# Optimization experiments

Hardware: AMD Instinct MI355X
Metric: run time of the kernel (lower is better)

## Reference

```python
import jax, jax.numpy as jnp
import numpy as np

B, N = 32, 2048
NUM_FEATURE, NUM_CLUSTER, D_MODEL = 512, 256, 1024
LN_EPS = 1e-5
NEG_SLOPE = 0.2


def setup_inputs() -> dict:
    key = jax.random.key(0)
    ks = jax.random.split(key, 8)
    s_feat = 1.0 / np.sqrt(NUM_FEATURE)
    s_city = 1.0 / np.sqrt(NUM_CLUSTER)
    return {
        "input": jax.random.normal(ks[0], (B, N, NUM_FEATURE), dtype=jnp.float32),
        "static": jax.random.normal(ks[1], (N, NUM_CLUSTER), dtype=jnp.float32),
        # torch.nn.Linear stores weight as [out, in]
        "W_feat": jax.random.uniform(ks[2], (D_MODEL, NUM_FEATURE), jnp.float32, -s_feat, s_feat),
        "b_feat": jax.random.uniform(ks[3], (D_MODEL,), jnp.float32, -s_feat, s_feat),
        "W_city": jax.random.uniform(ks[4], (D_MODEL, NUM_CLUSTER), jnp.float32, -s_city, s_city),
        "b_city": jax.random.uniform(ks[5], (D_MODEL,), jnp.float32, -s_city, s_city),
        "gamma": jnp.ones((D_MODEL,), dtype=jnp.float32),
        "beta": jnp.zeros((D_MODEL,), dtype=jnp.float32),
    }


def reference(input, static, W_feat, b_feat, W_city, b_city, gamma, beta):
    # x = leaky_relu(feat_embed(input), 0.2)  -> [B, N, d_model]
    x = jnp.einsum("bnf,df->bnd", input, W_feat) + b_feat
    x = jnp.where(x >= 0, x, NEG_SLOPE * x)
    # c = city_embed(static) -> [N, d_model]; diag_embed + matmul == elementwise gate
    c = jnp.einsum("nk,dk->nd", static, W_city) + b_city
    x = x * c[None, :, :]
    # LayerNorm over d_model (eps=1e-5, elementwise affine)
    mu = jnp.mean(x, axis=-1, keepdims=True)
    var = jnp.mean(jnp.square(x - mu), axis=-1, keepdims=True)
    x = (x - mu) * jax.lax.rsqrt(var + LN_EPS)
    return x * gamma + beta
```

## Files before the change

kernel.cpp:

```cpp
#include <hip/hip_runtime.h>
#include <hip/hip_bf16.h>


typedef __attribute__((ext_vector_type(8))) short short8;
typedef __attribute__((ext_vector_type(4))) float f32x4;

__device__ __forceinline__ unsigned short f2bf(float f) {
    unsigned int u = __float_as_uint(f);
    return (unsigned short)((u + 0x7FFFu + ((u >> 16) & 1u)) >> 16);
}
__device__ __forceinline__ float b2f(unsigned short h) {
    return __uint_as_float(((unsigned int)h) << 16);
}

__global__ __launch_bounds__(256) void convw_kernel(
    const float* __restrict__ w, unsigned short* __restrict__ o)
{
    int gid = blockIdx.x * 256 + threadIdx.x;
    int idx = gid * 4;
    int row = idx >> 9;
    int k   = idx & 511;
    float4 v = *(const float4*)(w + idx);
    uint2 p;
    p.x = (unsigned)f2bf(v.x) | ((unsigned)f2bf(v.y) << 16);
    p.y = (unsigned)f2bf(v.z) | ((unsigned)f2bf(v.w) << 16);
    int dst = ((k >> 5) << 15) + (row << 5) + (k & 31);
    *(uint2*)(o + dst) = p;
}

__global__ __launch_bounds__(256) void city_kernel(
    const float* __restrict__ st,
    const float* __restrict__ Wc,
    const float* __restrict__ bc,
    unsigned short* __restrict__ cg)
{
    __shared__ __align__(16) unsigned short Sa[64 * 264];
    __shared__ __align__(16) unsigned short Sb[128 * 264];
    const int t  = threadIdx.x;
    const int n0 = blockIdx.x << 6;
    const int d0 = blockIdx.y << 7;

    #pragma unroll
    for (int i = 0; i < 16; ++i) {
        int idx = (i << 8) + t;
        int row = idx >> 6, kq = (idx & 63) << 2;
        float4 v = *(const float4*)(st + (size_t)(n0 + row) * 256 + kq);
        uint2 p;
        p.x = (unsigned)f2bf(v.x) | ((unsigned)f2bf(v.y) << 16);
        p.y = (unsigned)f2bf(v.z) | ((unsigned)f2bf(v.w) << 16);
        *(uint2*)(Sa + row * 264 + kq) = p;
    }
    #pragma unroll
    for (int i = 0; i < 32; ++i) {
        int idx = (i << 8) + t;
        int row = idx >> 6, kq = (idx & 63) << 2;
        float4 v = *(const float4*)(Wc + (size_t)(d0 + row) * 256 + kq);
        uint2 p;
        p.x = (unsigned)f2bf(v.x) | ((unsigned)f2bf(v.y) << 16);
        p.y = (unsigned)f2bf(v.z) | ((unsigned)f2bf(v.w) << 16);
        *(uint2*)(Sb + row * 264 + kq) = p;
    }
    __syncthreads();

    const int wv = t >> 6;
    const int cl = t & 15, q = (t >> 4) & 3;
    f32x4 acc[4][2];
    #pragma unroll
    for (int rt = 0; rt < 4; ++rt)
        #pragma unroll
        for (int ct = 0; ct < 2; ++ct) acc[rt][ct] = (f32x4)0.f;

    #pragma unroll
    for (int ks = 0; ks < 8; ++ks) {
        short8 a[4];
        #pragma unroll
        for (int rt = 0; rt < 4; ++rt)
            a[rt] = *(const short8*)(Sa + ((rt << 4) + cl) * 264 + (ks << 5) + (q << 3));
        #pragma unroll
        for (int ct = 0; ct < 2; ++ct) {
            short8 bf8 = *(const short8*)(Sb + ((wv << 5) + (ct << 4) + cl) * 264 + (ks << 5) + (q << 3));
            #pragma unroll
            for (int rt = 0; rt < 4; ++rt)
                acc[rt][ct] = __builtin_amdgcn_mfma_f32_16x16x32_bf16(a[rt], bf8, acc[rt][ct], 0, 0, 0);
        }
    }
    #pragma unroll
    for (int ct = 0; ct < 2; ++ct) {
        const int d = d0 + (wv << 5) + (ct << 4) + cl;
        const float bcv = bc[d];
        #pragma unroll
        for (int rt = 0; rt < 4; ++rt)
            #pragma unroll
            for (int rr = 0; rr < 4; ++rr) {
                const int row = (rt << 4) + (q << 2) + rr;
                cg[(size_t)(n0 + row) * 1024 + d] = f2bf(acc[rt][ct][rr] + bcv);
            }
    }
}

__global__ __launch_bounds__(1024, 4) void feat_kernel(
    const float* __restrict__ inp,
    const unsigned short* __restrict__ Wr,
    const float* __restrict__ b_feat,
    const unsigned short* __restrict__ cg,
    const float* __restrict__ gamma,
    const float* __restrict__ beta,
    float* __restrict__ out)
{
    __shared__ __align__(16) unsigned short As[64 * 520];
    __shared__ float red1[16 * 64];
    __shared__ float red2[16 * 64];
    __shared__ float smu[64];
    __shared__ float srs[64];

    const int t    = threadIdx.x;
    const int lane = t & 63;
    const int w    = t >> 6;
    const int cl   = lane & 15;
    const int q    = lane >> 4;
    const int m0   = blockIdx.x << 6;
    const int n0   = m0 & 2047;

    f32x4 acc[4][4];
    #pragma unroll
    for (int rt = 0; rt < 4; ++rt)
        #pragma unroll
        for (int ct = 0; ct < 4; ++ct) acc[rt][ct] = (f32x4)0.f;

    const unsigned short* bp = Wr + ((((w << 6) + cl) << 5) + (q << 3));

    short8 bc[4], bn[4];
    #pragma unroll
    for (int ct = 0; ct < 4; ++ct)
        bc[ct] = *(const short8*)(bp + (ct << 9));

    {
        const float* ag = inp + (size_t)m0 * 512;
        #pragma unroll
        for (int j = 0; j < 8; ++j) {
            int g = (j << 10) + t;
            float4 v = *(const float4*)(ag + ((size_t)g << 2));
            int row = g >> 7, c4 = g & 127;
            uint2 p;
            p.x = (unsigned)f2bf(v.x) | ((unsigned)f2bf(v.y) << 16);
            p.y = (unsigned)f2bf(v.z) | ((unsigned)f2bf(v.w) << 16);
            *(uint2*)(&As[row * 520 + (c4 << 2)]) = p;
        }
    }
    __syncthreads();

    const int abase = cl * 520 + (q << 3);
    #pragma unroll
    for (int kb = 0; kb < 16; ++kb) {
        if (kb < 15) {
            #pragma unroll
            for (int ct = 0; ct < 4; ++ct)
                bn[ct] = *(const short8*)(bp + ((kb + 1) << 15) + (ct << 9));
        }
        short8 a[4];
        #pragma unroll
        for (int rt = 0; rt < 4; ++rt)
            a[rt] = *(const short8*)(&As[abase + rt * (16 * 520) + (kb << 5)]);
        #pragma unroll
        for (int ct = 0; ct < 4; ++ct)
            #pragma unroll
            for (int rt = 0; rt < 4; ++rt)
                acc[rt][ct] = __builtin_amdgcn_mfma_f32_16x16x32_bf16(a[rt], bc[ct], acc[rt][ct], 0, 0, 0);
        if (kb < 15) {
            #pragma unroll
            for (int ct = 0; ct < 4; ++ct) bc[ct] = bn[ct];
        }
    }

    float bfv[4];
    #pragma unroll
    for (int ct = 0; ct < 4; ++ct) bfv[ct] = b_feat[(w << 6) + (ct << 4) + cl];

    #pragma unroll
    for (int rt = 0; rt < 4; ++rt) {
        #pragma unroll
        for (int rr = 0; rr < 4; ++rr) {
            const int row = (rt << 4) + (q << 2) + rr;
            float s1 = 0.f, s2 = 0.f;
            #pragma unroll
            for (int ct = 0; ct < 4; ++ct) {
                const int d = (w << 6) + (ct << 4) + cl;
                float x = acc[rt][ct][rr] + bfv[ct];
                x = (x >= 0.f) ? x : 0.2f * x;
                x *= b2f(cg[(size_t)(n0 + row) * 1024 + d]);
                acc[rt][ct][rr] = x;
                s1 += x;
                s2 += x * x;
            }
            #pragma unroll
            for (int off = 1; off < 16; off <<= 1) {
                s1 += __shfl_xor(s1, off, 64);
                s2 += __shfl_xor(s2, off, 64);
            }
            if (cl == 0) {
                red1[(w << 6) + row] = s1;
                red2[(w << 6) + row] = s2;
            }
        }
    }
    __syncthreads();
    if (t < 64) {
        float a = 0.f, bb = 0.f;
        #pragma unroll
        for (int j = 0; j < 16; ++j) { a += red1[(j << 6) + t]; bb += red2[(j << 6) + t]; }
        const float mu  = a * (1.0f / 1024.0f);
        const float var = bb * (1.0f / 1024.0f) - mu * mu;
        smu[t] = mu;
        srs[t] = rsqrtf(var + 1e-5f);
    }
    __syncthreads();

    #pragma unroll
    for (int ct = 0; ct < 4; ++ct) {
        const int d = (w << 6) + (ct << 4) + cl;
        const float g = gamma[d], be = beta[d];
        #pragma unroll
        for (int rt = 0; rt < 4; ++rt) {
            #pragma unroll
            for (int rr = 0; rr < 4; ++rr) {
                const int row = (rt << 4) + (q << 2) + rr;
                __builtin_nontemporal_store(
                    (acc[rt][ct][rr] - smu[row]) * srs[row] * g + be,
                    &out[(size_t)(m0 + row) * 1024 + d]);
            }
        }
    }
}

extern "C" void kernel_launch(void* const* d_in, const int* in_sizes, int n_in,
                              void* d_out, int out_size, void* d_ws, size_t ws_size,
                              hipStream_t stream) {
    const float* inp   = (const float*)d_in[0];
    const float* st    = (const float*)d_in[1];
    const float* Wf    = (const float*)d_in[2];
    const float* bfeat = (const float*)d_in[3];
    const float* Wc    = (const float*)d_in[4];
    const float* bc    = (const float*)d_in[5];
    const float* gamma = (const float*)d_in[6];
    const float* beta  = (const float*)d_in[7];
    float* out = (float*)d_out;

    unsigned short* wsWr = (unsigned short*)d_ws;
    unsigned short* wsC  = (unsigned short*)((char*)d_ws + (1 << 20));

    convw_kernel<<<512, 256, 0, stream>>>(Wf, wsWr);
    city_kernel<<<dim3(32, 8), 256, 0, stream>>>(st, Wc, bc, wsC);
    feat_kernel<<<1024, 1024, 0, stream>>>(inp, wsWr, bfeat, wsC, gamma, beta, out);
}
```

Baseline: 486.2 us.

## Double-buffer A and W tiles in LDS via async global_load_lds

The feat kernel no longer converts the whole 64x512 input tile to bf16 in LDS up front, and no longer prefetches W through registers. It now streams both the fp32 input chunk and the bf16 weight chunk per k-step into double-buffered LDS using the asynchronous global_load_lds builtin, with an XOR-swizzled layout for the A tile. The fp32 to bf16 conversion of A moves into the inner loop, using packed convert instructions. The aim is to overlap global loads with MFMA work and to cut the serial prologue. In exchange it adds a block barrier every k-step, repeats A conversion across all 16 waves, and uses far more LDS (about 144KB), which limits occupancy to one block per CU.

Result: slower. 529.6 us (+8.9%).

```diff
diff --git a/kernel.cpp b/kernel.cpp
--- a/kernel.cpp
+++ b/kernel.cpp
@@ -12,6 +12,10 @@
 __device__ __forceinline__ float b2f(unsigned short h) {
     return __uint_as_float(((unsigned int)h) << 16);
 }
+
+#define LDS_ASYNC16(g, l) __builtin_amdgcn_global_load_lds(                 \
+    (const __attribute__((address_space(1))) void*)(g),                     \
+    (__attribute__((address_space(3))) void*)(l), 16, 0, 0)
 
 __global__ __launch_bounds__(256) void convw_kernel(
     const float* __restrict__ w, unsigned short* __restrict__ o)
@@ -107,9 +111,10 @@
     const float* __restrict__ beta,
     float* __restrict__ out)
 {
-    __shared__ __align__(16) unsigned short As[64 * 520];
-    __shared__ float red1[16 * 64];
-    __shared__ float red2[16 * 64];
+    __shared__ __align__(16) float          Ab[2][2048];
+    __shared__ __align__(16) unsigned short Bb[2][32768];
+    __shared__ float red1[1024];
+    __shared__ float red2[1024];
     __shared__ float smu[64];
     __shared__ float srs[64];
 
@@ -127,50 +132,61 @@
         #pragma unroll
         for (int ct = 0; ct < 4; ++ct) acc[rt][ct] = (f32x4)0.f;
 
-    const unsigned short* bp = Wr + ((((w << 6) + cl) << 5) + (q << 3));
-
-    short8 bc[4], bn[4];
-    #pragma unroll
-    for (int ct = 0; ct < 4; ++ct)
-        bc[ct] = *(const short8*)(bp + (ct << 9));
-
-    {
-        const float* ag = inp + (size_t)m0 * 512;
-        #pragma unroll
-        for (int j = 0; j < 8; ++j) {
-            int g = (j << 10) + t;
-            float4 v = *(const float4*)(ag + ((size_t)g << 2));
-            int row = g >> 7, c4 = g & 127;
-            uint2 p;
-            p.x = (unsigned)f2bf(v.x) | ((unsigned)f2bf(v.y) << 16);
-            p.y = (unsigned)f2bf(v.z) | ((unsigned)f2bf(v.w) << 16);
-            *(uint2*)(&As[row * 520 + (c4 << 2)]) = p;
-        }
-    }
-    __syncthreads();
-
-    const int abase = cl * 520 + (q << 3);
-    #pragma unroll
-    for (int kb = 0; kb < 16; ++kb) {
-        if (kb < 15) {
-            #pragma unroll
-            for (int ct = 0; ct < 4; ++ct)
-                bn[ct] = *(const short8*)(bp + ((kb + 1) << 15) + (ct << 9));
-        }
+    const unsigned short* bgp = Wr + (size_t)(lane << 3);
+    const int arow = (w << 3) + (lane >> 3);
+    const int acg  = (lane & 7) ^ (lane >> 3);
+    const float* agp = inp + (size_t)(m0 + arow) * 512 + (acg << 2);
+
+    const int key = cl & 7;
+    const int c0s = (((q << 1)) ^ key) << 2;
+    const int c1s = (((q << 1) | 1) ^ key) << 2;
+
+#define STAGE(pb, kb)                                                        \
+    do {                                                                     \
+        _Pragma("unroll")                                                    \
+        for (int j_ = 0; j_ < 4; ++j_) {                                     \
+            int i_ = (w << 2) + j_;                                          \
+            LDS_ASYNC16(bgp + ((size_t)(kb) << 15) + (i_ << 9),              \
+                        &Bb[pb][i_ << 9]);                                   \
+        }                                                                    \
+        if (w < 8)                                                           \
+            LDS_ASYNC16(agp + ((kb) << 5), &Ab[pb][w << 8]);                 \
+    } while (0)
+
+    STAGE(0, 0);
+    __syncthreads();
+
+    #pragma unroll
+    for (int ks = 0; ks < 16; ++ks) {
+        const int p = ks & 1;
+        if (ks < 15) STAGE(p ^ 1, ks + 1);
+
         short8 a[4];
         #pragma unroll
-        for (int rt = 0; rt < 4; ++rt)
-            a[rt] = *(const short8*)(&As[abase + rt * (16 * 520) + (kb << 5)]);
-        #pragma unroll
-        for (int ct = 0; ct < 4; ++ct)
+        for (int rt = 0; rt < 4; ++rt) {
+            const float* abase = &Ab[p][((rt << 4) + cl) << 5];
+            float4 lo = *(const float4*)(abase + c0s);
+            float4 hi = *(const float4*)(abase + c1s);
+            unsigned p0, p1, p2, p3;
+            asm("v_cvt_pk_bf16_f32 %0, %1, %2" : "=v"(p0) : "v"(lo.x), "v"(lo.y));
+            asm("v_cvt_pk_bf16_f32 %0, %1, %2" : "=v"(p1) : "v"(lo.z), "v"(lo.w));
+            asm("v_cvt_pk_bf16_f32 %0, %1, %2" : "=v"(p2) : "v"(hi.x), "v"(hi.y));
+            asm("v_cvt_pk_bf16_f32 %0, %1, %2" : "=v"(p3) : "v"(hi.z), "v"(hi.w));
+            union { unsigned u[4]; short8 s; } cv;
+            cv.u[0] = p0; cv.u[1] = p1; cv.u[2] = p2; cv.u[3] = p3;
+            a[rt] = cv.s;
+        }
+        #pragma unroll
+        for (int ct = 0; ct < 4; ++ct) {
+            short8 bf8 = *(const short8*)(
+                &Bb[p][(((w << 6) + (ct << 4) + cl) << 5) + (q << 3)]);
             #pragma unroll
             for (int rt = 0; rt < 4; ++rt)
-                acc[rt][ct] = __builtin_amdgcn_mfma_f32_16x16x32_bf16(a[rt], bc[ct], acc[rt][ct], 0, 0, 0);
-        if (kb < 15) {
-            #pragma unroll
-            for (int ct = 0; ct < 4; ++ct) bc[ct] = bn[ct];
-        }
-    }
+                acc[rt][ct] = __builtin_amdgcn_mfma_f32_16x16x32_bf16(a[rt], bf8, acc[rt][ct], 0, 0, 0);
+        }
+        __syncthreads();
+    }
+#undef STAGE
 
     float bfv[4];
     #pragma unroll
```
